# Optimization experiments

Hardware: AMD Instinct MI355X
Metric: run time of the kernel (lower is better)

## Reference

```python
import jax, jax.numpy as jnp
import numpy as np

N, E, B = 10000, 160000, 64
ND, ED, H, L, C = 128, 64, 256, 4, 10
LN_EPS = 1e-5


def _layernorm(x, g, b):
    mu = jnp.mean(x, axis=-1, keepdims=True)
    var = jnp.mean(jnp.square(x - mu), axis=-1, keepdims=True)
    return (x - mu) * jax.lax.rsqrt(var + LN_EPS) * g + b


def setup_inputs() -> dict:
    key = jax.random.key(0)
    ks = jax.random.split(key, 24)

    def w(k, shape, fan_in):
        return jax.random.normal(k, shape, jnp.float32) * (1.0 / np.sqrt(fan_in))

    node_features = jax.random.normal(ks[0], (N, ND), jnp.float32)
    edge_index = jax.random.randint(ks[1], (2, E), 0, N, jnp.int64)
    edge_features = jax.random.normal(ks[2], (E, ED), jnp.float32)
    # deterministic sorted batch assignment (no empty graphs)
    batch = (jnp.arange(N, dtype=jnp.int64) * B) // N

    inp = dict(
        node_features=node_features,
        edge_index=edge_index,
        edge_features=edge_features,
        batch=batch,
        node_W=w(ks[3], (ND, H), ND), node_b=jnp.zeros((H,), jnp.float32),
        edge_W=w(ks[4], (ED, H), ED), edge_b=jnp.zeros((H,), jnp.float32),
        msg_W1=w(ks[5], (L, 3 * H, H), 3 * H), msg_b1=jnp.zeros((L, H), jnp.float32),
        msg_W2=w(ks[6], (L, H, H), H), msg_b2=jnp.zeros((L, H), jnp.float32),
        upd_W1=w(ks[7], (L, 2 * H, H), 2 * H), upd_b1=jnp.zeros((L, H), jnp.float32),
        upd_W2=w(ks[8], (L, H, H), H), upd_b2=jnp.zeros((L, H), jnp.float32),
        ln_g=jnp.ones((L, H), jnp.float32), ln_b=jnp.zeros((L, H), jnp.float32),
        ro_W1=w(ks[9], (H, H), H), ro_b1=jnp.zeros((H,), jnp.float32),
        ro_W2=w(ks[10], (H, C), H), ro_b2=jnp.zeros((C,), jnp.float32),
    )
    return inp


def _forward(node_features, edge_features, node_W, node_b, edge_W, edge_b,
             msg_W1, msg_b1, msg_W2, msg_b2, upd_W1, upd_b1, upd_W2, upd_b2,
             ln_g, ln_b, ro_W1, ro_b1, ro_W2, ro_b2, edge_index, batch):
    src, dst = edge_index[0], edge_index[1]
    x = node_features @ node_W + node_b            # [N, H]
    edge_attr = edge_features @ edge_W + edge_b    # [E, H]
    for l in range(L):
        # batched gather-MLP over all edges (vectorized version of the per-edge loop)
        m_in = jnp.concatenate([x[src], x[dst], edge_attr], axis=-1)  # [E, 3H]
        msg = jax.nn.relu(m_in @ msg_W1[l] + msg_b1[l]) @ msg_W2[l] + msg_b2[l]
        agg = jnp.zeros_like(x).at[dst].add(msg)    # scatter-add by destination
        u_in = jnp.concatenate([x, agg], axis=-1)   # [N, 2H]
        upd = jax.nn.relu(u_in @ upd_W1[l] + upd_b1[l]) @ upd_W2[l] + upd_b2[l]
        x = _layernorm(x + upd, ln_g[l], ln_b[l])
    # global mean pool per graph
    sums = jax.ops.segment_sum(x, batch, num_segments=B)
    cnts = jax.ops.segment_sum(jnp.ones((x.shape[0], 1), x.dtype), batch, num_segments=B)
    pooled = sums / cnts                            # [B, H]
    return jax.nn.relu(pooled @ ro_W1 + ro_b1) @ ro_W2 + ro_b2  # [B, C]


def reference(node_features, edge_index, edge_features, batch,
              node_W, node_b, edge_W, edge_b,
              msg_W1, msg_b1, msg_W2, msg_b2,
              upd_W1, upd_b1, upd_W2, upd_b2,
              ln_g, ln_b, ro_W1, ro_b1, ro_W2, ro_b2):
    return _forward(node_features, edge_features, node_W, node_b, edge_W, edge_b,
                    msg_W1, msg_b1, msg_W2, msg_b2, upd_W1, upd_b1, upd_W2, upd_b2,
                    ln_g, ln_b, ro_W1, ro_b1, ro_W2, ro_b2, edge_index, batch)
```

## Files before the change

kernel.cpp:

```cpp
#include <hip/hip_runtime.h>
#include <cstdint>
#include <cstddef>


typedef unsigned short u16;
typedef __attribute__((ext_vector_type(4))) float f32x4;
typedef __attribute__((ext_vector_type(8))) short bf16x8;
typedef __attribute__((ext_vector_type(4))) short s16x4;

constexpr int kN  = 10000;
constexpr int kE  = 160000;
constexpr int kB  = 64;
constexpr int kH  = 256;
constexpr int kL  = 4;
constexpr int kC  = 10;
constexpr float kEps = 1e-5f;

struct __align__(16) F4 { float v[4]; };
__device__ __forceinline__ F4 ldF4(const float* p) { return *reinterpret_cast<const F4*>(p); }

__device__ __forceinline__ u16 f2bf(float f) {
    unsigned u = __builtin_bit_cast(unsigned, f);
    return (u16)((u + 0x7fffu + ((u >> 16) & 1u)) >> 16);
}
__device__ __forceinline__ float bf2f(u16 h) {
    return __builtin_bit_cast(float, (unsigned)h << 16);
}
__device__ __forceinline__ unsigned cvtpk(float lo, float hi) {
    unsigned r;
    asm("v_cvt_pk_bf16_f32 %0, %1, %2" : "=v"(r) : "v"(lo), "v"(hi));
    return r;
}

typedef __attribute__((address_space(1))) void GV;
typedef __attribute__((address_space(3))) void LV;
__device__ __forceinline__ void gl_lds16(const void* g, void* l) {
    __builtin_amdgcn_global_load_lds((GV*)g, (LV*)l, 16, 0, 0);
}
__device__ __forceinline__ void dma_w16k(const u16* __restrict__ Wc, char* lds, int tid) {
    const int w = tid >> 6, lane = tid & 63;
    char* lb = lds + w * 4096;
    const char* gb = (const char*)Wc + w * 4096 + lane * 16;
    #pragma unroll
    for (int i = 0; i < 4; ++i) gl_lds16(gb + i * 1024, lb + i * 1024);
}

__device__ __forceinline__ bf16x8 g_frag(const u16* __restrict__ g, int n, int kg) {
    return *reinterpret_cast<const bf16x8*>(g + n * 32 + ((kg ^ ((n >> 1) & 3)) << 3));
}
__device__ __forceinline__ bf16x8 rdfrag(const char* lds, int n, int kg) {
    return *reinterpret_cast<const bf16x8*>(lds + n * 64 + ((kg ^ ((n >> 1) & 3)) << 4));
}
__device__ __forceinline__ bf16x8 rdH(const char* H, int row, int kbyte) {
    return *reinterpret_cast<const bf16x8*>(H + row * 512 + (kbyte ^ ((row & 7) << 4)));
}

__global__ void k_detect_i64(const unsigned* __restrict__ w, int* __restrict__ flag) {
    if (threadIdx.x == 0 && blockIdx.x == 0) {
        int is64 = 1;
        for (int i = 0; i < 64; ++i)
            if (w[2*i + 1] != 0u) { is64 = 0; break; }
        *flag = is64;
    }
}
__global__ void k_cvt_idx(const unsigned* __restrict__ w, const int* __restrict__ flag,
                          int* __restrict__ out, int n) {
    int i = blockIdx.x * 256 + threadIdx.x;
    if (i < n) out[i] = (*flag) ? (int)w[2*i] : (int)w[i];
}

__global__ __launch_bounds__(256) void k_hist(const int* __restrict__ dst,
                                              int* __restrict__ cnt) {
    int e = blockIdx.x * 256 + threadIdx.x;
    if (e < kE) atomicAdd(&cnt[dst[e]], 1);
}
__global__ __launch_bounds__(256) void k_scan(const int* __restrict__ cnt,
                                              int* __restrict__ cur) {
    __shared__ int part[256];
    const int t = threadIdx.x;
    const int per = (kN + 255) / 256;
    int s = 0;
    for (int i = 0; i < per; ++i) {
        int idx = t * per + i;
        if (idx < kN) s += cnt[idx];
    }
    int own = s;
    part[t] = s; __syncthreads();
    for (int off = 1; off < 256; off <<= 1) {
        int v = (t >= off) ? part[t - off] : 0;
        __syncthreads();
        part[t] += v;
        __syncthreads();
    }
    int run = part[t] - own;
    for (int i = 0; i < per; ++i) {
        int idx = t * per + i;
        if (idx < kN) { cur[idx] = run; run += cnt[idx]; }
    }
}
__global__ __launch_bounds__(256) void k_scatter(
    const int* __restrict__ src, const int* __restrict__ dst,
    int* __restrict__ cur, int* __restrict__ rank,
    int* __restrict__ ssorted, int* __restrict__ dsorted) {
    int e = blockIdx.x * 256 + threadIdx.x;
    if (e < kE) {
        int d = dst[e];
        int p = atomicAdd(&cur[d], 1);
        rank[e] = p;
        ssorted[p] = src[e];
        dsorted[p] = d;
    }
}

__global__ __launch_bounds__(256) void k_prep_w(
    const float* __restrict__ mW1, const float* __restrict__ mW2,
    const float* __restrict__ uW1, const float* __restrict__ uW2,
    u16* __restrict__ tm1, u16* __restrict__ tm2,
    u16* __restrict__ tu1, u16* __restrict__ tu2)
{
    int idx = blockIdx.x * 256 + threadIdx.x;
    const int S1 = kL * 768 * 256;
    const int S2 = S1 + kL * 256 * 256;
    const int S3 = S2 + kL * 512 * 256;
    const int S4 = S3 + kL * 256 * 256;
    const float* src; u16* dst; int K, r;
    if (idx < S1)      { src = mW1; dst = tm1; K = 768; r = idx; }
    else if (idx < S2) { src = mW2; dst = tm2; K = 256; r = idx - S1; }
    else if (idx < S3) { src = uW1; dst = tu1; K = 512; r = idx - S2; }
    else if (idx < S4) { src = uW2; dst = tu2; K = 256; r = idx - S3; }
    else return;
    int per = K * 256;
    int layer = r / per, rr = r - layer * per;
    int k = rr >> 8, n = rr & 255;
    int kc = k >> 5, kg = (k >> 3) & 3, e = k & 7;
    dst[(size_t)layer * per + (size_t)kc * 8192 + n * 32 + ((kg ^ ((n >> 1) & 3)) << 3) + e]
        = f2bf(src[(size_t)layer * per + rr]);
}

__global__ __launch_bounds__(256) void k_prep_ef(
    const float* __restrict__ ef, const int* __restrict__ rank,
    u16* __restrict__ efs)
{
    int idx = blockIdx.x * 256 + threadIdx.x;
    if (idx >= kE * 64) return;
    int e = idx >> 6, k = idx & 63;
    float v = ef[idx];
    int p = rank[e];
    int row = p & 63, blk = p >> 6;
    int kc = k >> 5, kg = (k >> 3) & 3, ee = k & 7;
    efs[(size_t)blk * 4096 + kc * 2048 + row * 32
        + ((kg ^ ((row >> 1) & 3)) << 3) + ee] = f2bf(v);
}

__global__ __launch_bounds__(256) void k_prep_m(
    const float* __restrict__ eW, const float* __restrict__ eb,
    const float* __restrict__ mW1, const float* __restrict__ mb1,
    u16* __restrict__ tmc, float* __restrict__ b1p)
{
    __shared__ float sWe[16 * 256];
    const int l = blockIdx.x, rq = blockIdx.y, t = threadIdx.x;
    const int r0 = rq * 16;
    #pragma unroll
    for (int i = 0; i < 16; ++i) sWe[i * 256 + t] = eW[(size_t)(r0 + i) * 256 + t];
    __syncthreads();
    const float* W1c = mW1 + (size_t)l * 768 * 256 + (size_t)512 * 256;
    float m[16];
    #pragma unroll
    for (int r = 0; r < 16; ++r) m[r] = 0.f;
    float bp = (rq == 0) ? mb1[l * 256 + t] : 0.f;
    for (int j = 0; j < 256; ++j) {
        float wv = W1c[(size_t)j * 256 + t];
        if (rq == 0) bp = fmaf(eb[j], wv, bp);
        #pragma unroll
        for (int r = 0; r < 16; ++r) m[r] = fmaf(sWe[r * 256 + j], wv, m[r]);
    }
    if (rq == 0) b1p[l * 256 + t] = bp;
    #pragma unroll
    for (int r = 0; r < 16; ++r) {
        int k = r0 + r;
        int kc = k >> 5, kg = (k >> 3) & 3, e = k & 7;
        tmc[(size_t)l * 16384 + (size_t)kc * 8192 + t * 32
            + ((kg ^ ((t >> 1) & 3)) << 3) + e] = f2bf(m[r]);
    }
}

__global__ __launch_bounds__(256) void k_encode_nodes(
    const float* __restrict__ nf, const float* __restrict__ W,
    const float* __restrict__ b, float* __restrict__ x, u16* __restrict__ x_bf)
{
    __shared__ float s_nf[4 * 128];
    const int n0 = blockIdx.x * 4;
    const int tid = threadIdx.x;
    reinterpret_cast<float2*>(s_nf)[tid] =
        reinterpret_cast<const float2*>(nf + (size_t)n0 * 128)[tid];
    __syncthreads();
    float acc[4] = {0.f, 0.f, 0.f, 0.f};
    for (int k = 0; k < 128; ++k) {
        float w = W[k * kH + tid];
        #pragma unroll
        for (int r = 0; r < 4; ++r) acc[r] = fmaf(s_nf[r * 128 + k], w, acc[r]);
    }
    float bias = b[tid];
    #pragma unroll
    for (int r = 0; r < 4; ++r) {
        float o = acc[r] + bias;
        x[(size_t)(n0 + r) * kH + tid] = o;
        x_bf[(size_t)(n0 + r) * kH + tid] = f2bf(o);
    }
}

__global__ __launch_bounds__(256, 3) void k_node_pre(
    const u16* __restrict__ x_bf, const u16* __restrict__ Wtm1,
    const u16* __restrict__ Wtu1,
    u16* __restrict__ y_a, u16* __restrict__ y_b, u16* __restrict__ y_c)
{
    __shared__ char sWt[16384];
    __shared__ char sA[4096];
    const int tid = threadIdx.x;
    const int n0 = blockIdx.x * 64;
    const int half = blockIdx.y;
    const u16* Wt = (half == 2) ? Wtu1 : Wtm1 + (size_t)half * 8 * 8192;
    u16* y = (half == 0) ? y_a : (half == 1 ? y_b : y_c);
    const int w = tid >> 6, lane = tid & 63;
    const int lr = lane & 15, lg = lane >> 4;
    const int srow = tid >> 2, skg = tid & 3;
    const int kg_src = skg ^ ((srow >> 1) & 3);
    int gnode = n0 + srow; if (gnode >= kN) gnode = kN - 1;

    f32x4 acc[4][4];
    #pragma unroll
    for (int i = 0; i < 4; ++i)
        #pragma unroll
        for (int j = 0; j < 4; ++j) acc[i][j] = (f32x4){0.f, 0.f, 0.f, 0.f};

    for (int kc = 0; kc < 8; ++kc) {
        __syncthreads();
        dma_w16k(Wt + (size_t)kc * 8192, sWt, tid);
        gl_lds16(x_bf + (size_t)gnode * kH + kc * 32 + kg_src * 8, sA + w * 1024);
        __syncthreads();
        bf16x8 af[4], bfm[4];
        #pragma unroll
        for (int i = 0; i < 4; ++i) af[i] = rdfrag(sWt, w * 64 + i * 16 + lr, lg);
        #pragma unroll
        for (int j = 0; j < 4; ++j) bfm[j] = rdfrag(sA, j * 16 + lr, lg);
        #pragma unroll
        for (int i = 0; i < 4; ++i)
            #pragma unroll
            for (int j = 0; j < 4; ++j)
                acc[i][j] = __builtin_amdgcn_mfma_f32_16x16x32_bf16(af[i], bfm[j], acc[i][j], 0, 0, 0);
    }
    #pragma unroll
    for (int i = 0; i < 4; ++i) {
        const int hc0 = w * 64 + i * 16 + lg * 4;
        #pragma unroll
        for (int j = 0; j < 4; ++j) {
            const int node = n0 + j * 16 + lr;
            if (node < kN) {
                uint2 o;
                o.x = cvtpk(acc[i][j][0], acc[i][j][1]);
                o.y = cvtpk(acc[i][j][2], acc[i][j][3]);
                *reinterpret_cast<uint2*>(y + (size_t)node * kH + hc0) = o;
            }
        }
    }
}

__global__ __launch_bounds__(256, 4) void k_msg(
    const u16* __restrict__ efs,
    const int* __restrict__ ssorted, const int* __restrict__ dsorted,
    const u16* __restrict__ y_a, const u16* __restrict__ y_b,
    const u16* __restrict__ Wtm, const float* __restrict__ b1p,
    const u16* __restrict__ Wt2, const float* __restrict__ b2,
    float* __restrict__ agg)
{
    __shared__ char sH[32768];
    __shared__ int sDst[64];

    const int tid = threadIdx.x;
    const int nwg = gridDim.x;
    const int q8 = nwg >> 3, r8 = nwg & 7;
    const int xcd = blockIdx.x & 7, sub = blockIdx.x >> 3;
    const int bid = (xcd < r8 ? xcd * (q8 + 1) : r8 * (q8 + 1) + (xcd - r8) * q8) + sub;
    const int e0 = bid * 64;

    const int w = tid >> 6, lane = tid & 63;
    const int lr = lane & 15, lg = lane >> 4;

    if (tid < 64) sDst[tid] = dsorted[e0 + tid];

    uint2 ya[4][4], yb[4][4];
    #pragma unroll
    for (int j = 0; j < 4; ++j) {
        const int es = ssorted[e0 + j * 16 + lr];
        const int ed = dsorted[e0 + j * 16 + lr];
        const u16* pa = y_a + (size_t)es * kH;
        const u16* pb = y_b + (size_t)ed * kH;
        #pragma unroll
        for (int i = 0; i < 4; ++i) {
            const int hc0 = w * 64 + i * 16 + lg * 4;
            ya[j][i] = *reinterpret_cast<const uint2*>(pa + hc0);
            yb[j][i] = *reinterpret_cast<const uint2*>(pb + hc0);
        }
    }

    f32x4 acc[4][4];
    #pragma unroll
    for (int i = 0; i < 4; ++i)
        #pragma unroll
        for (int j = 0; j < 4; ++j) acc[i][j] = (f32x4){0.f, 0.f, 0.f, 0.f};

    #pragma unroll
    for (int kc = 0; kc < 2; ++kc) {
        const u16* efc = efs + (size_t)bid * 4096 + kc * 2048;
        bf16x8 af[4], bfm[4];
        #pragma unroll
        for (int i = 0; i < 4; ++i) af[i] = g_frag(Wtm + kc * 8192, w * 64 + i * 16 + lr, lg);
        #pragma unroll
        for (int j = 0; j < 4; ++j) {
            int row = j * 16 + lr;
            bfm[j] = *reinterpret_cast<const bf16x8*>(
                efc + row * 32 + ((lg ^ ((row >> 1) & 3)) << 3));
        }
        #pragma unroll
        for (int i = 0; i < 4; ++i)
            #pragma unroll
            for (int j = 0; j < 4; ++j)
                acc[i][j] = __builtin_amdgcn_mfma_f32_16x16x32_bf16(af[i], bfm[j], acc[i][j], 0, 0, 0);
    }

    #pragma unroll
    for (int j = 0; j < 4; ++j) {
        const int edge = j * 16 + lr;
        #pragma unroll
        for (int i = 0; i < 4; ++i) {
            const int hc0 = w * 64 + i * 16 + lg * 4;
            const F4 bb = ldF4(b1p + hc0);
            float s0 = __builtin_bit_cast(float, ya[j][i].x << 16) + __builtin_bit_cast(float, yb[j][i].x << 16);
            float s1 = __builtin_bit_cast(float, ya[j][i].x & 0xffff0000u) + __builtin_bit_cast(float, yb[j][i].x & 0xffff0000u);
            float s2 = __builtin_bit_cast(float, ya[j][i].y << 16) + __builtin_bit_cast(float, yb[j][i].y << 16);
            float s3 = __builtin_bit_cast(float, ya[j][i].y & 0xffff0000u) + __builtin_bit_cast(float, yb[j][i].y & 0xffff0000u);
            float h0 = acc[i][j][0] + bb.v[0] + s0; h0 = h0 > 0.f ? h0 : 0.f;
            float h1 = acc[i][j][1] + bb.v[1] + s1; h1 = h1 > 0.f ? h1 : 0.f;
            float h2 = acc[i][j][2] + bb.v[2] + s2; h2 = h2 > 0.f ? h2 : 0.f;
            float h3 = acc[i][j][3] + bb.v[3] + s3; h3 = h3 > 0.f ? h3 : 0.f;
            uint2 o; o.x = cvtpk(h0, h1); o.y = cvtpk(h2, h3);
            int byte = edge * 512 + hc0 * 2;
            *reinterpret_cast<uint2*>(sH + (byte ^ ((edge & 7) << 4))) = o;
            acc[i][j] = (f32x4){0.f, 0.f, 0.f, 0.f};
        }
    }
    __syncthreads();

    #pragma unroll 2
    for (int kc = 0; kc < 8; ++kc) {
        bf16x8 af2[4], bf2[4];
        #pragma unroll
        for (int i = 0; i < 4; ++i) af2[i] = rdH(sH, i * 16 + lr, kc * 64 + lg * 16);
        #pragma unroll
        for (int j = 0; j < 4; ++j) bf2[j] = g_frag(Wt2 + kc * 8192, w * 64 + j * 16 + lr, lg);
        #pragma unroll
        for (int i = 0; i < 4; ++i)
            #pragma unroll
            for (int j = 0; j < 4; ++j)
                acc[i][j] = __builtin_amdgcn_mfma_f32_16x16x32_bf16(af2[i], bf2[j], acc[i][j], 0, 0, 0);
    }

    __syncthreads();
    #pragma unroll
    for (int j = 0; j < 4; ++j) {
        const int oc = w * 64 + j * 16 + lr;
        const float b2v = b2[oc];
        #pragma unroll
        for (int i = 0; i < 4; ++i) {
            unsigned p01 = cvtpk(acc[i][j][0] + b2v, acc[i][j][1] + b2v);
            unsigned p23 = cvtpk(acc[i][j][2] + b2v, acc[i][j][3] + b2v);
            int eb0 = i * 16 + lg * 4;
            *reinterpret_cast<u16*>(sH + (((eb0 + 0) * 512 + oc * 2) ^ (((eb0 + 0) & 7) << 4))) = (u16)p01;
            *reinterpret_cast<u16*>(sH + (((eb0 + 1) * 512 + oc * 2) ^ (((eb0 + 1) & 7) << 4))) = (u16)(p01 >> 16);
            *reinterpret_cast<u16*>(sH + (((eb0 + 2) * 512 + oc * 2) ^ (((eb0 + 2) & 7) << 4))) = (u16)p23;
            *reinterpret_cast<u16*>(sH + (((eb0 + 3) * 512 + oc * 2) ^ (((eb0 + 3) & 7) << 4))) = (u16)(p23 >> 16);
        }
    }
    __syncthreads();

    {
        const int col = tid;
        float run = 0.f;
        int prev = sDst[0];
        #pragma unroll 1
        for (int eb = 0; eb < 8; ++eb) {
            float vv[8]; int dd[8];
            #pragma unroll
            for (int t = 0; t < 8; ++t) {
                int e = eb * 8 + t;
                int byte = e * 512 + col * 2;
                vv[t] = bf2f(*reinterpret_cast<const u16*>(sH + (byte ^ ((e & 7) << 4))));
                dd[t] = sDst[e];
            }
            #pragma unroll
            for (int t = 0; t < 8; ++t) {
                if (dd[t] != prev) {
                    unsafeAtomicAdd(agg + (size_t)prev * kH + col, run);
                    run = 0.f; prev = dd[t];
                }
                run += vv[t];
            }
        }
        unsafeAtomicAdd(agg + (size_t)prev * kH + col, run);
    }
}

__global__ __launch_bounds__(256, 3) void k_upd(
    float* __restrict__ x, u16* __restrict__ x_bf,
    float* __restrict__ agg,
    const u16* __restrict__ Wt1b, const float* __restrict__ b1,
    const u16* __restrict__ Wt2, const float* __restrict__ b2,
    const float* __restrict__ lng, const float* __restrict__ lnb,
    const u16* __restrict__ y_c)
{
    __shared__ char sWt[2][16384];
    __shared__ char sA[2][2048];
    __shared__ char sH[16384];

    const int tid = threadIdx.x;
    const int n0 = blockIdx.x * 32;
    const int w = tid >> 6, lane = tid & 63;
    const int lr = lane & 15, lg = lane >> 4;
    const int srow = tid >> 2, skg = tid & 3;
    int gnode = n0 + (srow & 31); if (gnode >= kN) gnode = kN - 1;
    const bool stg = tid < 128;

    f32x4 acc[4][4];
    #pragma unroll
    for (int i = 0; i < 4; ++i)
        #pragma unroll
        for (int j = 0; j < 4; ++j) acc[i][j] = (f32x4){0.f, 0.f, 0.f, 0.f};

    dma_w16k(Wt1b, sWt[0], tid);
    if (stg) {
        const float* ap = agg + (size_t)gnode * kH + skg * 8;
        F4 a0 = ldF4(ap), a1 = ldF4(ap + 4);
        int4 bv;
        bv.x = (int)cvtpk(a0.v[0], a0.v[1]);
        bv.y = (int)cvtpk(a0.v[2], a0.v[3]);
        bv.z = (int)cvtpk(a1.v[0], a1.v[1]);
        bv.w = (int)cvtpk(a1.v[2], a1.v[3]);
        *reinterpret_cast<int4*>(sA[0] + srow * 64 + ((skg ^ ((srow >> 1) & 3)) << 4)) = bv;
    }
    __syncthreads();

    for (int kc = 0; kc < 8; ++kc) {
        const int cur = kc & 1, nxt = cur ^ 1;
        bool pf = false; F4 a0, a1;
        if (kc < 7) {
            dma_w16k(Wt1b + (size_t)(kc + 1) * 8192, sWt[nxt], tid);
            if (stg) {
                const float* ap = agg + (size_t)gnode * kH + (kc + 1) * 32 + skg * 8;
                a0 = ldF4(ap); a1 = ldF4(ap + 4); pf = true;
            }
        } else {
            dma_w16k(Wt2, sWt[nxt], tid);
        }
        bf16x8 af[4], bfm[2];
        #pragma unroll
        for (int i = 0; i < 4; ++i) af[i] = rdfrag(sWt[cur], w * 64 + i * 16 + lr, lg);
        #pragma unroll
        for (int j = 0; j < 2; ++j) bfm[j] = rdfrag(sA[cur], j * 16 + lr, lg);
        #pragma unroll
        for (int i = 0; i < 4; ++i)
            #pragma unroll
            for (int j = 0; j < 2; ++j)
                acc[i][j] = __builtin_amdgcn_mfma_f32_16x16x32_bf16(af[i], bfm[j], acc[i][j], 0, 0, 0);
        if (pf) {
            int4 bv;
            bv.x = (int)cvtpk(a0.v[0], a0.v[1]);
            bv.y = (int)cvtpk(a0.v[2], a0.v[3]);
            bv.z = (int)cvtpk(a1.v[0], a1.v[1]);
            bv.w = (int)cvtpk(a1.v[2], a1.v[3]);
            *reinterpret_cast<int4*>(sA[nxt] + srow * 64 + ((skg ^ ((srow >> 1) & 3)) << 4)) = bv;
        }
        __syncthreads();
    }

    #pragma unroll
    for (int i = 0; i < 4; ++i) {
        const int hc0 = w * 64 + i * 16 + lg * 4;
        const F4 bb = ldF4(b1 + hc0);
        #pragma unroll
        for (int j = 0; j < 2; ++j) {
            const int row = j * 16 + lr;
            int ncl = n0 + row; if (ncl >= kN) ncl = kN - 1;
            uint2 yc = *reinterpret_cast<const uint2*>(y_c + (size_t)ncl * kH + hc0);
            float s0 = __builtin_bit_cast(float, yc.x << 16);
            float s1 = __builtin_bit_cast(float, yc.x & 0xffff0000u);
            float s2 = __builtin_bit_cast(float, yc.y << 16);
            float s3 = __builtin_bit_cast(float, yc.y & 0xffff0000u);
            float h0 = acc[i][j][0] + bb.v[0] + s0; h0 = h0 > 0.f ? h0 : 0.f;
            float h1 = acc[i][j][1] + bb.v[1] + s1; h1 = h1 > 0.f ? h1 : 0.f;
            float h2 = acc[i][j][2] + bb.v[2] + s2; h2 = h2 > 0.f ? h2 : 0.f;
            float h3 = acc[i][j][3] + bb.v[3] + s3; h3 = h3 > 0.f ? h3 : 0.f;
            uint2 o; o.x = cvtpk(h0, h1); o.y = cvtpk(h2, h3);
            int byte = row * 512 + hc0 * 2;
            *reinterpret_cast<uint2*>(sH + (byte ^ ((row & 7) << 4))) = o;
            acc[i][j] = (f32x4){0.f, 0.f, 0.f, 0.f};
        }
    }
    __syncthreads();

    {
        float4 z = make_float4(0.f, 0.f, 0.f, 0.f);
        float4* bp = reinterpret_cast<float4*>(agg + (size_t)n0 * kH);
        #pragma unroll
        for (int i = 0; i < 8; ++i) {
            int idx = i * 256 + tid;
            int row = idx >> 6;
            if (n0 + row < kN) bp[idx] = z;
        }
    }

    for (int kc = 0; kc < 8; ++kc) {
        const int cur = kc & 1, nxt = cur ^ 1;
        if (kc < 7) dma_w16k(Wt2 + (size_t)(kc + 1) * 8192, sWt[nxt], tid);
        bf16x8 af2[2], bf2[4];
        #pragma unroll
        for (int i = 0; i < 2; ++i) af2[i] = rdH(sH, i * 16 + lr, kc * 64 + lg * 16);
        #pragma unroll
        for (int j = 0; j < 4; ++j) bf2[j] = rdfrag(sWt[cur], w * 64 + j * 16 + lr, lg);
        #pragma unroll
        for (int i = 0; i < 2; ++i)
            #pragma unroll
            for (int j = 0; j < 4; ++j)
                acc[i][j] = __builtin_amdgcn_mfma_f32_16x16x32_bf16(af2[i], bf2[j], acc[i][j], 0, 0, 0);
        __syncthreads();
    }

    float b2v[4], gv[4], bvn[4];
    #pragma unroll
    for (int j = 0; j < 4; ++j) {
        int oc = w * 64 + j * 16 + lr;
        b2v[j] = b2[oc]; gv[j] = lng[oc]; bvn[j] = lnb[oc];
    }
    #pragma unroll
    for (int i = 0; i < 2; ++i)
        #pragma unroll
        for (int j = 0; j < 4; ++j) {
            int oc = w * 64 + j * 16 + lr;
            #pragma unroll
            for (int q = 0; q < 4; ++q) {
                int node = n0 + i * 16 + lg * 4 + q;
                int ncl = node < kN ? node : kN - 1;
                acc[i][j][q] += b2v[j] + x[(size_t)ncl * kH + oc];
            }
        }

    float (*red)[32][2] = reinterpret_cast<float(*)[32][2]>(sA[0]);
    float2* mstd = reinterpret_cast<float2*>((char*)sA[0] + 1024);
    #pragma unroll
    for (int i = 0; i < 2; ++i)
        #pragma unroll
        for (int q = 0; q < 4; ++q) {
            float s = acc[i][0][q] + acc[i][1][q] + acc[i][2][q] + acc[i][3][q];
            float ss = acc[i][0][q] * acc[i][0][q] + acc[i][1][q] * acc[i][1][q]
                     + acc[i][2][q] * acc[i][2][q] + acc[i][3][q] * acc[i][3][q];
            #pragma unroll
            for (int m = 1; m < 16; m <<= 1) { s += __shfl_xor(s, m); ss += __shfl_xor(ss, m); }
            if (lr == 0) { red[w][i * 16 + lg * 4 + q][0] = s; red[w][i * 16 + lg * 4 + q][1] = ss; }
        }
    __syncthreads();
    if (tid < 32) {
        float s = red[0][tid][0] + red[1][tid][0] + red[2][tid][0] + red[3][tid][0];
        float ss = red[0][tid][1] + red[1][tid][1] + red[2][tid][1] + red[3][tid][1];
        float mean = s * (1.f / 256.f);
        float var = ss * (1.f / 256.f) - mean * mean;
        mstd[tid] = make_float2(mean, rsqrtf(var + kEps));
    }
    __syncthreads();
    #pragma unroll
    for (int i = 0; i < 2; ++i)
        #pragma unroll
        for (int j = 0; j < 4; ++j) {
            int oc = w * 64 + j * 16 + lr;
            #pragma unroll
            for (int q = 0; q < 4; ++q) {
                int nn = i * 16 + lg * 4 + q;
                int node = n0 + nn;
                if (node < kN) {
                    float2 ms = mstd[nn];
                    float o = (acc[i][j][q] - ms.x) * ms.y * gv[j] + bvn[j];
                    x[(size_t)node * kH + oc] = o;
                    x_bf[(size_t)node * kH + oc] = f2bf(o);
                }
            }
        }
}

__device__ __forceinline__ int lower_bound_i(const int* a, int n, int v) {
    int lo = 0, hi = n;
    while (lo < hi) { int m = (lo + hi) >> 1; if (a[m] < v) lo = m + 1; else hi = m; }
    return lo;
}

__global__ __launch_bounds__(256) void k_pool_part(
    const float* __restrict__ x, const int* __restrict__ batch,
    float* __restrict__ pooled)
{
    const int b = blockIdx.x >> 2, q = blockIdx.x & 3, t = threadIdx.x;
    const int s = lower_bound_i(batch, kN, b);
    const int e = lower_bound_i(batch, kN, b + 1);
    const int len = e - s;
    const int qs = s + (len * q) / 4;
    const int qe = s + (len * (q + 1)) / 4;
    float acc = 0.f;
    for (int i = qs; i < qe; ++i) acc += x[(size_t)i * kH + t];
    unsafeAtomicAdd(pooled + b * kH + t, acc);
}

__global__ __launch_bounds__(256) void k_ro(
    const float* __restrict__ pooled, const int* __restrict__ batch,
    const float* __restrict__ W1, const float* __restrict__ b1,
    const float* __restrict__ W2, const float* __restrict__ b2,
    float* __restrict__ out)
{
    __shared__ float ph[kH];
    __shared__ float h1[kH];
    const int b = blockIdx.x, t = threadIdx.x;
    const int s = lower_bound_i(batch, kN, b);
    const int e = lower_bound_i(batch, kN, b + 1);
    ph[t] = pooled[b * kH + t] / (float)(e - s);
    __syncthreads();
    float a = b1[t];
    for (int k = 0; k < kH; ++k) a = fmaf(ph[k], W1[k * kH + t], a);
    h1[t] = a > 0.f ? a : 0.f;
    __syncthreads();
    if (t < kC) {
        float o = b2[t];
        for (int k = 0; k < kH; ++k) o = fmaf(h1[k], W2[k * kC + t], o);
        out[b * kC + t] = o;
    }
}

extern "C" void kernel_launch(void* const* d_in, const int* in_sizes, int n_in,
                              void* d_out, int out_size, void* d_ws, size_t ws_size,
                              hipStream_t stream)
{
    const float* nf     = (const float*)d_in[0];
    const void*  ei_raw = d_in[1];
    const float* ef     = (const float*)d_in[2];
    const void*  ba_raw = d_in[3];
    const float* node_W = (const float*)d_in[4];
    const float* node_b = (const float*)d_in[5];
    const float* edge_W = (const float*)d_in[6];
    const float* edge_b = (const float*)d_in[7];
    const float* msg_W1 = (const float*)d_in[8];
    const float* msg_b1 = (const float*)d_in[9];
    const float* msg_W2 = (const float*)d_in[10];
    const float* msg_b2 = (const float*)d_in[11];
    const float* upd_W1 = (const float*)d_in[12];
    const float* upd_b1 = (const float*)d_in[13];
    const float* upd_W2 = (const float*)d_in[14];
    const float* upd_b2 = (const float*)d_in[15];
    const float* ln_g   = (const float*)d_in[16];
    const float* ln_b   = (const float*)d_in[17];
    const float* ro_W1  = (const float*)d_in[18];
    const float* ro_b1  = (const float*)d_in[19];
    const float* ro_W2  = (const float*)d_in[20];
    const float* ro_b2  = (const float*)d_in[21];

    char* p = (char*)d_ws;
    auto alloc = [&](size_t bytes) { char* r = p; p += (bytes + 255) & ~(size_t)255; return r; };
    float* x    = (float*)alloc((size_t)kN * kH * 4);
    float* agg  = (float*)alloc((size_t)kN * kH * 4);
    float* pooled = (float*)alloc((size_t)kB * kH * 4);
    u16* x_bf   = (u16*)alloc((size_t)kN * kH * 2);
    u16* y_a    = (u16*)alloc((size_t)kN * kH * 2);
    u16* y_b    = (u16*)alloc((size_t)kN * kH * 2);
    u16* y_c    = (u16*)alloc((size_t)kN * kH * 2);
    u16* efs    = (u16*)alloc((size_t)kE * 64 * 2);
    u16* tm1 = (u16*)alloc((size_t)kL * 768 * 256 * 2);
    u16* tm2 = (u16*)alloc((size_t)kL * 256 * 256 * 2);
    u16* tu1 = (u16*)alloc((size_t)kL * 512 * 256 * 2);
    u16* tu2 = (u16*)alloc((size_t)kL * 256 * 256 * 2);
    u16* tmc = (u16*)alloc((size_t)kL * 64 * 256 * 2);
    float* b1p = (float*)alloc((size_t)kL * 256 * 4);
    int* ei32 = (int*)alloc((size_t)2 * kE * 4);
    int* ba32 = (int*)alloc((size_t)kN * 4);
    int* cnt  = (int*)alloc((size_t)kN * 4);
    int* cur  = (int*)alloc((size_t)kN * 4);
    int* rank = (int*)alloc((size_t)kE * 4);
    int* ssorted = (int*)alloc((size_t)kE * 4);
    int* dsorted = (int*)alloc((size_t)kE * 4);
    int* flag = (int*)alloc(4);

    k_detect_i64<<<1, 64, 0, stream>>>((const unsigned*)ei_raw, flag);
    k_cvt_idx<<<(2 * kE + 255) / 256, 256, 0, stream>>>((const unsigned*)ei_raw, flag, ei32, 2 * kE);
    k_cvt_idx<<<(kN + 255) / 256, 256, 0, stream>>>((const unsigned*)ba_raw, flag, ba32, kN);
    const int* src = ei32;
    const int* dst = ei32 + kE;

    hipMemsetAsync(cnt, 0, (size_t)kN * 4, stream);
    k_hist<<<(kE + 255) / 256, 256, 0, stream>>>(dst, cnt);
    k_scan<<<1, 256, 0, stream>>>(cnt, cur);
    k_scatter<<<(kE + 255) / 256, 256, 0, stream>>>(src, dst, cur, rank, ssorted, dsorted);

    const int prep_elems = kL * (768 + 256 + 512 + 256) * 256;
    k_prep_w<<<(prep_elems + 255) / 256, 256, 0, stream>>>(
        msg_W1, msg_W2, upd_W1, upd_W2, tm1, tm2, tu1, tu2);
    k_prep_m<<<dim3(kL, 4), 256, 0, stream>>>(edge_W, edge_b, msg_W1, msg_b1, tmc, b1p);
    k_prep_ef<<<(kE * 64 + 255) / 256, 256, 0, stream>>>(ef, rank, efs);

    k_encode_nodes<<<kN / 4, 256, 0, stream>>>(nf, node_W, node_b, x, x_bf);
    hipMemsetAsync(agg, 0, (size_t)kN * kH * sizeof(float), stream);
    hipMemsetAsync(pooled, 0, (size_t)kB * kH * sizeof(float), stream);

    for (int l = 0; l < kL; ++l) {
        k_node_pre<<<dim3((kN + 63) / 64, 3), 256, 0, stream>>>(
            x_bf, tm1 + (size_t)l * 768 * 256, tu1 + (size_t)l * 512 * 256,
            y_a, y_b, y_c);
        k_msg<<<kE / 64, 256, 0, stream>>>(efs, ssorted, dsorted, y_a, y_b,
            tmc + (size_t)l * 64 * 256, b1p + l * 256,
            tm2 + (size_t)l * 256 * 256, msg_b2 + l * kH, agg);
        k_upd<<<(kN + 31) / 32, 256, 0, stream>>>(x, x_bf, agg,
            tu1 + (size_t)l * 512 * 256 + 8 * 8192, upd_b1 + l * kH,
            tu2 + (size_t)l * 256 * 256, upd_b2 + l * kH,
            ln_g + l * kH, ln_b + l * kH, y_c);
    }

    k_pool_part<<<kB * 4, 256, 0, stream>>>(x, ba32, pooled);
    k_ro<<<kB, 256, 0, stream>>>(pooled, ba32, ro_W1, ro_b1, ro_W2, ro_b2, (float*)d_out);
}
```

Before: 555.8 us.

## Double-buffer node_pre loads, transpose msg scatter staging, prefetch y_c in upd

k_node_pre now double-buffers its weight and activation tiles in LDS, so the next K chunk loads while the current one runs MFMAs, and it needs one barrier per iteration instead of two. k_msg writes its second-GEMM output to a column-major padded LDS layout with vector stores. The segmented scatter then reads it with 16-byte loads and uses a ballot mask of destination boundaries instead of comparing destinations per element. k_upd issues its y_c loads at kernel start to hide their latency behind the GEMM, at the cost of more registers held live and more LDS in node_pre, which may lower occupancy.

```diff
diff --git a/kernel.cpp b/kernel.cpp
--- a/kernel.cpp
+++ b/kernel.cpp
@@ -214,8 +214,8 @@
     const u16* __restrict__ Wtu1,
     u16* __restrict__ y_a, u16* __restrict__ y_b, u16* __restrict__ y_c)
 {
-    __shared__ char sWt[16384];
-    __shared__ char sA[4096];
+    __shared__ char sWt[2][16384];
+    __shared__ char sA[2][4096];
     const int tid = threadIdx.x;
     const int n0 = blockIdx.x * 64;
     const int half = blockIdx.y;
@@ -233,21 +233,28 @@
         #pragma unroll
         for (int j = 0; j < 4; ++j) acc[i][j] = (f32x4){0.f, 0.f, 0.f, 0.f};
 
+    dma_w16k(Wt, sWt[0], tid);
+    gl_lds16(x_bf + (size_t)gnode * kH + kg_src * 8, sA[0] + w * 1024);
+    __syncthreads();
+
     for (int kc = 0; kc < 8; ++kc) {
-        __syncthreads();
-        dma_w16k(Wt + (size_t)kc * 8192, sWt, tid);
-        gl_lds16(x_bf + (size_t)gnode * kH + kc * 32 + kg_src * 8, sA + w * 1024);
-        __syncthreads();
+        const int cur = kc & 1, nxt = cur ^ 1;
+        if (kc < 7) {
+            dma_w16k(Wt + (size_t)(kc + 1) * 8192, sWt[nxt], tid);
+            gl_lds16(x_bf + (size_t)gnode * kH + (kc + 1) * 32 + kg_src * 8,
+                     sA[nxt] + w * 1024);
+        }
         bf16x8 af[4], bfm[4];
         #pragma unroll
-        for (int i = 0; i < 4; ++i) af[i] = rdfrag(sWt, w * 64 + i * 16 + lr, lg);
-        #pragma unroll
-        for (int j = 0; j < 4; ++j) bfm[j] = rdfrag(sA, j * 16 + lr, lg);
+        for (int i = 0; i < 4; ++i) af[i] = rdfrag(sWt[cur], w * 64 + i * 16 + lr, lg);
+        #pragma unroll
+        for (int j = 0; j < 4; ++j) bfm[j] = rdfrag(sA[cur], j * 16 + lr, lg);
         #pragma unroll
         for (int i = 0; i < 4; ++i)
             #pragma unroll
             for (int j = 0; j < 4; ++j)
                 acc[i][j] = __builtin_amdgcn_mfma_f32_16x16x32_bf16(af[i], bfm[j], acc[i][j], 0, 0, 0);
+        __syncthreads();
     }
     #pragma unroll
     for (int i = 0; i < 4; ++i) {
@@ -273,8 +280,9 @@
     const u16* __restrict__ Wt2, const float* __restrict__ b2,
     float* __restrict__ agg)
 {
-    __shared__ char sH[32768];
+    __shared__ __align__(16) char sBuf[36864];
     __shared__ int sDst[64];
+    __shared__ unsigned long long sMask;
 
     const int tid = threadIdx.x;
     const int nwg = gridDim.x;
@@ -345,7 +353,7 @@
             float h3 = acc[i][j][3] + bb.v[3] + s3; h3 = h3 > 0.f ? h3 : 0.f;
             uint2 o; o.x = cvtpk(h0, h1); o.y = cvtpk(h2, h3);
             int byte = edge * 512 + hc0 * 2;
-            *reinterpret_cast<uint2*>(sH + (byte ^ ((edge & 7) << 4))) = o;
+            *reinterpret_cast<uint2*>(sBuf + (byte ^ ((edge & 7) << 4))) = o;
             acc[i][j] = (f32x4){0.f, 0.f, 0.f, 0.f};
         }
     }
@@ -355,7 +363,7 @@
     for (int kc = 0; kc < 8; ++kc) {
         bf16x8 af2[4], bf2[4];
         #pragma unroll
-        for (int i = 0; i < 4; ++i) af2[i] = rdH(sH, i * 16 + lr, kc * 64 + lg * 16);
+        for (int i = 0; i < 4; ++i) af2[i] = rdH(sBuf, i * 16 + lr, kc * 64 + lg * 16);
         #pragma unroll
         for (int j = 0; j < 4; ++j) bf2[j] = g_frag(Wt2 + kc * 8192, w * 64 + j * 16 + lr, lg);
         #pragma unroll
@@ -364,49 +372,52 @@
             for (int j = 0; j < 4; ++j)
                 acc[i][j] = __builtin_amdgcn_mfma_f32_16x16x32_bf16(af2[i], bf2[j], acc[i][j], 0, 0, 0);
     }
-
-    __syncthreads();
+    __syncthreads();
+
     #pragma unroll
     for (int j = 0; j < 4; ++j) {
         const int oc = w * 64 + j * 16 + lr;
         const float b2v = b2[oc];
         #pragma unroll
         for (int i = 0; i < 4; ++i) {
-            unsigned p01 = cvtpk(acc[i][j][0] + b2v, acc[i][j][1] + b2v);
-            unsigned p23 = cvtpk(acc[i][j][2] + b2v, acc[i][j][3] + b2v);
-            int eb0 = i * 16 + lg * 4;
-            *reinterpret_cast<u16*>(sH + (((eb0 + 0) * 512 + oc * 2) ^ (((eb0 + 0) & 7) << 4))) = (u16)p01;
-            *reinterpret_cast<u16*>(sH + (((eb0 + 1) * 512 + oc * 2) ^ (((eb0 + 1) & 7) << 4))) = (u16)(p01 >> 16);
-            *reinterpret_cast<u16*>(sH + (((eb0 + 2) * 512 + oc * 2) ^ (((eb0 + 2) & 7) << 4))) = (u16)p23;
-            *reinterpret_cast<u16*>(sH + (((eb0 + 3) * 512 + oc * 2) ^ (((eb0 + 3) & 7) << 4))) = (u16)(p23 >> 16);
-        }
+            uint2 o;
+            o.x = cvtpk(acc[i][j][0] + b2v, acc[i][j][1] + b2v);
+            o.y = cvtpk(acc[i][j][2] + b2v, acc[i][j][3] + b2v);
+            *reinterpret_cast<uint2*>(sBuf + oc * 144 + i * 32 + lg * 8) = o;
+        }
+    }
+    if (tid < 64) {
+        int flag = (tid == 63) || (sDst[tid] != sDst[tid + 1]);
+        unsigned long long m = __ballot(flag);
+        if (tid == 0) sMask = m;
     }
     __syncthreads();
 
     {
         const int col = tid;
+        unsigned long long msk = sMask;
+        unsigned mlo = __builtin_amdgcn_readfirstlane((unsigned)(msk & 0xffffffffu));
+        unsigned mhi = __builtin_amdgcn_readfirstlane((unsigned)(msk >> 32));
         float run = 0.f;
-        int prev = sDst[0];
-        #pragma unroll 1
-        for (int eb = 0; eb < 8; ++eb) {
-            float vv[8]; int dd[8];
+        #pragma unroll
+        for (int e8 = 0; e8 < 8; ++e8) {
+            uint4 v = *reinterpret_cast<const uint4*>(sBuf + col * 144 + e8 * 16);
+            unsigned wv[4] = {v.x, v.y, v.z, v.w};
             #pragma unroll
             for (int t = 0; t < 8; ++t) {
-                int e = eb * 8 + t;
-                int byte = e * 512 + col * 2;
-                vv[t] = bf2f(*reinterpret_cast<const u16*>(sH + (byte ^ ((e & 7) << 4))));
-                dd[t] = sDst[e];
+                const int e = e8 * 8 + t;
+                unsigned u = wv[t >> 1];
+                float val = (t & 1)
+                    ? __builtin_bit_cast(float, u & 0xffff0000u)
+                    : __builtin_bit_cast(float, u << 16);
+                run += val;
+                unsigned mm = (e < 32) ? mlo : mhi;
+                if ((mm >> (e & 31)) & 1u) {
+                    unsafeAtomicAdd(agg + (size_t)sDst[e] * kH + col, run);
+                    run = 0.f;
+                }
             }
-            #pragma unroll
-            for (int t = 0; t < 8; ++t) {
-                if (dd[t] != prev) {
-                    unsafeAtomicAdd(agg + (size_t)prev * kH + col, run);
-                    run = 0.f; prev = dd[t];
-                }
-                run += vv[t];
-            }
-        }
-        unsafeAtomicAdd(agg + (size_t)prev * kH + col, run);
+        }
     }
 }
 
@@ -429,6 +440,17 @@
     const int srow = tid >> 2, skg = tid & 3;
     int gnode = n0 + (srow & 31); if (gnode >= kN) gnode = kN - 1;
     const bool stg = tid < 128;
+
+    uint2 ycv[4][2];
+    #pragma unroll
+    for (int i = 0; i < 4; ++i) {
+        const int hc0 = w * 64 + i * 16 + lg * 4;
+        #pragma unroll
+        for (int j = 0; j < 2; ++j) {
+            int ncl = n0 + j * 16 + lr; if (ncl >= kN) ncl = kN - 1;
+            ycv[i][j] = *reinterpret_cast<const uint2*>(y_c + (size_t)ncl * kH + hc0);
+        }
+    }
 
     f32x4 acc[4][4];
     #pragma unroll
@@ -489,12 +511,10 @@
         #pragma unroll
         for (int j = 0; j < 2; ++j) {
             const int row = j * 16 + lr;
-            int ncl = n0 + row; if (ncl >= kN) ncl = kN - 1;
-            uint2 yc = *reinterpret_cast<const uint2*>(y_c + (size_t)ncl * kH + hc0);
-            float s0 = __builtin_bit_cast(float, yc.x << 16);
-            float s1 = __builtin_bit_cast(float, yc.x & 0xffff0000u);
-            float s2 = __builtin_bit_cast(float, yc.y << 16);
-            float s3 = __builtin_bit_cast(float, yc.y & 0xffff0000u);
+            float s0 = __builtin_bit_cast(float, ycv[i][j].x << 16);
+            float s1 = __builtin_bit_cast(float, ycv[i][j].x & 0xffff0000u);
+            float s2 = __builtin_bit_cast(float, ycv[i][j].y << 16);
+            float s3 = __builtin_bit_cast(float, ycv[i][j].y & 0xffff0000u);
             float h0 = acc[i][j][0] + bb.v[0] + s0; h0 = h0 > 0.f ? h0 : 0.f;
             float h1 = acc[i][j][1] + bb.v[1] + s1; h1 = h1 > 0.f ? h1 : 0.f;
             float h2 = acc[i][j][2] + bb.v[2] + s2; h2 = h2 > 0.f ? h2 : 0.f;
```

Result: no change. 557.3 us (+0.3%).
